# Kernel optimization log

Hardware: AMD Instinct MI355X
Metric: run time of the kernel (lower is better)

The kernel has to match this reference:

```python
import jax, jax.numpy as jnp
import numpy as np
import itertools

M_MODES = 16      # optical modes
N_PHOTONS = 8     # photons, input_state = [1]*8 + [0]*8
N_STATES = 12870  # C(16, 8) no-bunching output Fock states
OUT_SIZE = 128
BATCH = 8


def _random_unitary(key, m):
    kr, ki = jax.random.split(key)
    z = jax.random.normal(kr, (m, m)) + 1j * jax.random.normal(ki, (m, m))
    q, _ = jnp.linalg.qr(z)
    return q.astype(jnp.complex64)


def setup_inputs() -> dict:
    key = jax.random.key(0)
    ks = jax.random.split(key, 8)
    x = jax.random.normal(ks[0], (BATCH, M_MODES), dtype=jnp.float32)
    theta1 = jax.random.normal(ks[1], (M_MODES,), dtype=jnp.float32) * jnp.pi
    theta2 = jax.random.normal(ks[2], (M_MODES,), dtype=jnp.float32) * jnp.pi
    # fixed passive mixing unitaries (circuit structure constants)
    mix = jnp.stack([_random_unitary(jax.random.fold_in(ks[3], i), M_MODES) for i in range(4)])
    m_real = mix.real.astype(jnp.float32)
    m_imag = mix.imag.astype(jnp.float32)
    weight = jax.random.normal(ks[4], (N_STATES, OUT_SIZE), dtype=jnp.float32) * 0.02
    bias = jnp.zeros((OUT_SIZE,), dtype=jnp.float32)
    # no-bunching output Fock basis: all C(16,8) mode subsets (sorted rows)
    rows_idx = jnp.asarray(np.array(list(itertools.combinations(range(M_MODES), N_PHOTONS)), dtype=np.int32))
    return {"x": x, "theta1": theta1, "theta2": theta2, "m_real": m_real,
            "m_imag": m_imag, "weight": weight, "bias": bias, "rows_idx": rows_idx}


def reference(x, theta1, theta2, m_real, m_imag, weight, bias, rows_idx):
    n = N_PHOTONS
    M = (m_real + 1j * m_imag).astype(jnp.complex64)  # [4, m, m]
    # circuit unitary: U(x) = M3 . D(theta2) . M2 . D(x) . M1 . D(theta1) . M0
    A = M[1] @ (jnp.exp(1j * theta1)[:, None] * M[0])        # [m, m]
    B = M[3] @ (jnp.exp(1j * theta2)[:, None] * M[2])        # [m, m]
    U = jnp.einsum('pm,bm,mn->bpn', B, jnp.exp(1j * x), A)   # [b, m, m]
    # photons enter the first n modes -> keep those columns
    Uin = U[:, :, :n]                                        # [b, m, n]
    # Ryser's permanent formula over all 2^n column subsets
    sub = jnp.arange(2 ** n)
    masks = ((sub[:, None] >> jnp.arange(n)[None, :]) & 1).astype(jnp.float32)  # [2^n, n]
    popc = masks.sum(-1)
    signs = jnp.where((popc % 2) == 0, 1.0, -1.0) * ((-1.0) ** n)               # [2^n]
    # row partial sums for every mode and subset
    V = jnp.einsum('bmn,sn->bms', Uin, masks.astype(jnp.complex64))             # [b, m, 2^n]
    # product over the n rows of each output state (small fixed loop, not a data loop)
    acc = V[:, rows_idx[:, 0], :]                            # [b, states, 2^n]
    for i in range(1, n):
        acc = acc * V[:, rows_idx[:, i], :]
    amps = jnp.einsum('bks,s->bk', acc, signs.astype(jnp.complex64))            # [b, states]
    probs = amps.real ** 2 + amps.imag ** 2
    probs = probs / jnp.sum(probs, axis=-1, keepdims=True)   # renormalize over no-bunching subspace
    return probs @ weight + bias                             # linear output mapping
```

## Files before the change

### kernel.cpp

```cpp
#include <hip/hip_runtime.h>
#include <math.h>

#define NB 8
#define NM 16
#define NPH 8
#define NSTATES 12870
#define NSUB 256
#define OUTS 128
#define NTILES 824
#define NSLOTS (NTILES*16)
#define NSG 16
#define SPH 16
#define NTG 4
#define TILES_PER_TG 206
#define NGRID 512
#define SLOTS_P2 32
#define NP2 412

struct Tables {
  int binom[17][9];
  unsigned char cls_masks[256];
  int cls_off[10];
  int nt1[9], nt2[9];
  int tile_off[10];
};

constexpr int cpopc(int x){ int c=0; while(x){ c += x & 1; x >>= 1; } return c; }

constexpr Tables make_tables(){
  Tables t{};
  for (int n=0;n<=16;n++)
    for (int k=0;k<=8;k++){
      if (k==0) t.binom[n][k]=1;
      else if (n==0) t.binom[n][k]=0;
      else t.binom[n][k]=t.binom[n-1][k-1]+t.binom[n-1][k];
    }
  int idx=0;
  for (int p=0;p<=8;p++){
    t.cls_off[p]=idx;
    for (int m=0;m<256;m++) if (cpopc(m)==p) t.cls_masks[idx++]=(unsigned char)m;
  }
  t.cls_off[9]=idx;
  int toff=0;
  for (int c=0;c<=8;c++){
    int R=t.binom[8][c], C=t.binom[8][8-c];
    t.nt1[c]=(R+3)/4; t.nt2[c]=(C+3)/4;
    t.tile_off[c]=toff; toff += t.nt1[c]*t.nt2[c];
  }
  t.tile_off[9]=toff;
  return t;
}

constexpr Tables HTBL = make_tables();
static_assert(HTBL.tile_off[9]==NTILES, "tile count");
static_assert(HTBL.cls_off[9]==256, "mask count");
__device__ const Tables TBL = HTBL;

#define WS_TMAP   0
#define WS_BSUM2  53248
#define WS_POUT2  66560
#define WS_PART   1754112

__device__ __forceinline__ float2 cmul(float2 a, float2 b){
  return make_float2(fmaf(a.x,b.x,-(a.y*b.y)), fmaf(a.x,b.y, a.y*b.x));
}
__device__ __forceinline__ void cmac(float2& acc, float2 a, float2 b){
  acc.x = fmaf(a.x, b.x, acc.x); acc.x = fmaf(-a.y, b.y, acc.x);
  acc.y = fmaf(a.x, b.y, acc.y); acc.y = fmaf(a.y, b.x, acc.y);
}

__global__ __launch_bounds__(256) void k_p1(
    const float* __restrict__ x, const float* __restrict__ th1,
    const float* __restrict__ th2, const float* __restrict__ mr,
    const float* __restrict__ mi, const int* __restrict__ rows, char* ws)
{
  __shared__ float2 P[32][256];
  float2* __restrict__ part = (float2*)(ws + WS_PART);
  int tid = threadIdx.x;
  int blk = blockIdx.x;
  int b = blk >> 6, rest = blk & 63, sg = rest >> 2, tg = rest & 3;
  int sbase = sg * SPH;

  float2 (*T1)[NM]  = reinterpret_cast<float2(*)[NM]>(P[0]);
  float2 (*T2)[NM]  = reinterpret_cast<float2(*)[NM]>(P[1]);
  float2 (*Am)[NM]  = reinterpret_cast<float2(*)[NM]>(P[2]);
  float2 (*Bm)[NM]  = reinterpret_cast<float2(*)[NM]>(P[3]);
  float2 (*EA)[NPH] = reinterpret_cast<float2(*)[NPH]>(P[4]);
  float2* exP = P[4] + 128;
  float2 (*UinL)[NPH] = reinterpret_cast<float2(*)[NPH]>(P[5]);

  {
    int r = tid >> 4, cc = tid & 15;
    float sn, cs;
    sincosf(th1[r], &sn, &cs);
    float a = mr[0*256 + tid], bb = mi[0*256 + tid];
    T1[r][cc] = make_float2(cs*a - sn*bb, cs*bb + sn*a);
    sincosf(th2[r], &sn, &cs);
    float a2 = mr[2*256 + tid], b2 = mi[2*256 + tid];
    T2[r][cc] = make_float2(cs*a2 - sn*b2, cs*b2 + sn*a2);
    if (tid < NM){ float s2, c2; sincosf(x[b*NM + tid], &s2, &c2); exP[tid] = make_float2(c2, s2); }
  }
  __syncthreads();
  {
    int r = tid >> 4, cc = tid & 15;
    float2 accA = make_float2(0,0), accB = make_float2(0,0);
    for (int m=0;m<NM;m++){
      float2 m1 = make_float2(mr[1*256 + r*16+m], mi[1*256 + r*16+m]);
      cmac(accA, m1, T1[m][cc]);
      float2 m3 = make_float2(mr[3*256 + r*16+m], mi[3*256 + r*16+m]);
      cmac(accB, m3, T2[m][cc]);
    }
    Am[r][cc] = accA; Bm[r][cc] = accB;
  }
  __syncthreads();
  if (tid < NM*NPH){ int m = tid >> 3, n = tid & 7; EA[m][n] = cmul(exP[m], Am[m][n]); }
  __syncthreads();
  if (tid < NM*NPH){
    int p = tid >> 3, n = tid & 7;
    float2 acc = make_float2(0,0);
    for (int m=0;m<NM;m++) cmac(acc, Bm[p][m], EA[m][n]);
    UinL[p][n] = acc;
  }
  __syncthreads();

  int ts = tid >> 3;
  int table = ts >> 4, sl = ts & 15;
  int sv = sbase + sl;
  float2 v[8];
  {
    #pragma unroll
    for (int j=0;j<8;j++){
      float2 a = make_float2(0,0);
      int m = table*8 + j;
      #pragma unroll
      for (int jj=0;jj<NPH;jj++)
        if ((sv>>jj) & 1){ a.x += UinL[m][jj].x; a.y += UinL[m][jj].y; }
      v[j] = a;
    }
  }
  __syncthreads();

  {
    int chunk = tid & 7;
    int t0 = chunk << 5;
    float2 ph = make_float2((table==0 && (__popc(sv)&1)) ? -1.0f : 1.0f, 0.0f);
    if (chunk & 4) ph = cmul(ph, v[7]);
    if (chunk & 2) ph = cmul(ph, v[6]);
    if (chunk & 1) ph = cmul(ph, v[5]);
    float2 p[32];
    p[0] = ph;
    #pragma unroll
    for (int u=1; u<32; u++){
      int par = u & (u-1);
      int lb = (u&1) ? 0 : ((u&2) ? 1 : ((u&4) ? 2 : ((u&8) ? 3 : 4)));
      p[u] = cmul(p[par], v[lb]);
    }
    int swz = (ts & 15) << 1;
    #pragma unroll
    for (int u=0; u<32; u+=2){
      int tc = (t0 + u) ^ swz;
      *(float4*)&P[ts][tc] = make_float4(p[u].x, p[u].y, p[u+1].x, p[u+1].y);
    }
  }

  bool active = tid < TILES_PER_TG;
  int tile = tg + 4*tid;
  int t1v[4] = {0,0,0,0}, t2v[4] = {0,0,0,0};
  if (active){
    int c = 0;
    while (tile >= TBL.tile_off[c+1]) c++;
    int local = tile - TBL.tile_off[c];
    int n2 = TBL.nt2[c];
    int ti = local / n2, tj = local - ti*n2;
    int R = TBL.binom[8][c], C2 = TBL.binom[8][8-c];
    #pragma unroll
    for (int i=0;i<4;i++){ int r1 = ti*4+i; t1v[i] = (r1<R) ? (int)TBL.cls_masks[TBL.cls_off[c]+r1] : 0; }
    #pragma unroll
    for (int j=0;j<4;j++){ int r2 = tj*4+j; t2v[j] = (r2<C2) ? (int)TBL.cls_masks[TBL.cls_off[8-c]+r2] : 0; }
  }
  __syncthreads();

  if (active){
    float2 acc[4][4] = {};
    for (int s=0;s<SPH;s++){
      int swz = s << 1;
      float2 av[4], bv[4];
      #pragma unroll
      for (int i=0;i<4;i++) av[i] = P[s][t1v[i] ^ swz];
      #pragma unroll
      for (int j=0;j<4;j++) bv[j] = P[16+s][t2v[j] ^ swz];
      #pragma unroll
      for (int i=0;i<4;i++)
        #pragma unroll
        for (int j=0;j<4;j++) cmac(acc[i][j], av[i], bv[j]);
    }
    float2* dst = part + (size_t)(b*NSG + sg)*NSLOTS + (size_t)tile*16;
    #pragma unroll
    for (int i=0;i<4;i++)
      #pragma unroll
      for (int j=0;j<4;j++) dst[i*4+j] = acc[i][j];
  }

  if (tg == 3){
    int idx = blk >> 2;
    int kb = idx * 101;
    int ke = min(NSTATES, kb + 101);
    int k = kb + tid;
    if (k < ke){
      int t1=0, t2=0;
      #pragma unroll
      for (int i=0;i<NPH;i++){
        int rr = rows[k*NPH+i];
        if (rr < 8) t1 |= 1 << rr; else t2 |= 1 << (rr-8);
      }
      int c1 = __popc(t1);
      int rk1=0, cnt=0;
      #pragma unroll
      for (int bb=0;bb<8;bb++) if ((t1>>bb)&1){ cnt++; rk1 += TBL.binom[bb][cnt]; }
      int rk2=0; cnt=0;
      #pragma unroll
      for (int bb=0;bb<8;bb++) if ((t2>>bb)&1){ cnt++; rk2 += TBL.binom[bb][cnt]; }
      int tl = TBL.tile_off[c1] + (rk1>>2)*TBL.nt2[c1] + (rk2>>2);
      int slot = ((rk1&3)<<2) | (rk2&3);
      ((int*)(ws + WS_TMAP))[tl*16 + slot] = k;
    }
  }
}

__global__ __launch_bounds__(256) void k_p2(const float* __restrict__ wgt, char* ws)
{
  __shared__ float prob[NB*SLOTS_P2];
  __shared__ int   krow[SLOTS_P2];
  __shared__ float hacc[2*NB*OUTS];
  int tid = threadIdx.x;
  int blk = blockIdx.x;
  int slot0 = blk * SLOTS_P2;

  if (tid < SLOTS_P2){
    int slot = slot0 + tid;
    int tile = slot >> 4;
    int c = 0;
    while (tile >= TBL.tile_off[c+1]) c++;
    int local = tile - TBL.tile_off[c];
    int n2 = TBL.nt2[c];
    int ti = local / n2, tj = local - ti*n2;
    int r1 = ti*4 + ((slot >> 2) & 3);
    int r2 = tj*4 + (slot & 3);
    bool pad = (r1 >= TBL.binom[8][c]) || (r2 >= TBL.binom[8][8-c]);
    krow[tid] = pad ? -1 : ((const int*)(ws + WS_TMAP))[slot];
  }
  __syncthreads();

  const float2* __restrict__ part = (const float2*)(ws + WS_PART);
  float* __restrict__ bsum2 = (float*)(ws + WS_BSUM2);
  {
    int b = tid >> 5, sl = tid & 31;
    float2 amp = make_float2(0,0);
    #pragma unroll
    for (int g=0; g<NSG; g++){
      float2 v = part[(size_t)(b*NSG + g)*NSLOTS + slot0 + sl];
      amp.x += v.x; amp.y += v.y;
    }
    float pr = (krow[sl] >= 0) ? fmaf(amp.x, amp.x, amp.y*amp.y) : 0.0f;
    prob[b*SLOTS_P2 + sl] = pr;
    float v = pr;
    #pragma unroll
    for (int off=16; off>0; off>>=1) v += __shfl_down(v, off, 32);
    if (sl == 0) bsum2[blk*NB + b] = v;
  }
  __syncthreads();

  {
    int h = tid >> 7, o = tid & 127;
    float acc[NB] = {0,0,0,0,0,0,0,0};
    int sbeg = h*16, send = sbeg + 16;
    #pragma unroll 4
    for (int sl = sbeg; sl < send; sl++){
      int kr = krow[sl]; if (kr < 0) kr = 0;
      float wv = wgt[(size_t)kr * OUTS + o];
      #pragma unroll
      for (int b=0;b<NB;b++) acc[b] = fmaf(prob[b*SLOTS_P2 + sl], wv, acc[b]);
    }
    #pragma unroll
    for (int b=0;b<NB;b++) hacc[h*(NB*OUTS) + b*OUTS + o] = acc[b];
  }
  __syncthreads();

  float* __restrict__ pout2 = (float*)(ws + WS_POUT2);
  for (int idx = tid; idx < NB*OUTS; idx += 256)
    pout2[(size_t)blk*(NB*OUTS) + idx] = hacc[idx] + hacc[NB*OUTS + idx];
}

__global__ __launch_bounds__(256) void k_p3(
    const float* __restrict__ bias, const char* __restrict__ ws,
    float* __restrict__ out)
{
  __shared__ float accs[2*OUTS];
  __shared__ float wred[4];
  int tid = threadIdx.x, b = blockIdx.x;
  const float* __restrict__ bsum2 = (const float*)(ws + WS_BSUM2);
  const float* __restrict__ pout2 = (const float*)(ws + WS_POUT2);

  float v = 0.0f;
  for (int j = tid; j < NP2; j += 256) v += bsum2[j*NB + b];
  #pragma unroll
  for (int off=32; off>0; off>>=1) v += __shfl_down(v, off);
  if ((tid & 63) == 0) wred[tid >> 6] = v;

  int o = tid & 127, half = tid >> 7;
  float a = 0.0f;
  #pragma unroll 4
  for (int s = half; s < NP2; s += 2) a += pout2[(size_t)s*(NB*OUTS) + b*OUTS + o];
  accs[half*OUTS + o] = a;
  __syncthreads();
  if (tid < OUTS){
    float norm = wred[0] + wred[1] + wred[2] + wred[3];
    out[b*OUTS + tid] = (accs[tid] + accs[OUTS + tid]) / norm + bias[tid];
  }
}

extern "C" void kernel_launch(void* const* d_in, const int* in_sizes, int n_in,
                              void* d_out, int out_size, void* d_ws, size_t ws_size,
                              hipStream_t stream) {
  const float* x    = (const float*)d_in[0];
  const float* th1  = (const float*)d_in[1];
  const float* th2  = (const float*)d_in[2];
  const float* mr   = (const float*)d_in[3];
  const float* mi   = (const float*)d_in[4];
  const float* wgt  = (const float*)d_in[5];
  const float* bias = (const float*)d_in[6];
  const int*   rows = (const int*)d_in[7];
  float* out = (float*)d_out;
  char* ws = (char*)d_ws;

  k_p1<<<NGRID, 256, 0, stream>>>(x, th1, th2, mr, mi, rows, ws);
  k_p2<<<NP2, 256, 0, stream>>>(wgt, ws);
  k_p3<<<NB, 256, 0, stream>>>(bias, ws, out);
}
```

Measured before the change: 121.0 us.

## Fuse final reduction into k_p2 via atomic counter, split product table

Removes the separate k_p3 launch. Every k_p2 block takes a ticket from a global atomic counter, which k_p1 resets. The last NB blocks to arrive spin until all blocks have finished, then each reduces one batch row into the output. Separately, k_p1 builds its 32-entry subset-product table as two halves of 16 values, to lower register pressure. The cost is a spin-wait at the tail of k_p2 and a dependence on inter-block memory ordering through fences.

```diff
diff --git a/kernel.cpp b/kernel.cpp
--- a/kernel.cpp
+++ b/kernel.cpp
@@ -16,6 +16,7 @@
 #define NGRID 512
 #define SLOTS_P2 32
 #define NP2 412
+#define FIN0 (NP2-NB)
 
 struct Tables {
   int binom[17][9];
@@ -56,10 +57,11 @@
 static_assert(HTBL.cls_off[9]==256, "mask count");
 __device__ const Tables TBL = HTBL;
 
-#define WS_TMAP   0
+#define WS_CNT    0
+#define WS_TMAP   256
 #define WS_BSUM2  53248
 #define WS_POUT2  66560
-#define WS_PART   1754112
+#define WS_PART   1757184
 
 __device__ __forceinline__ float2 cmul(float2 a, float2 b){
   return make_float2(fmaf(a.x,b.x,-(a.y*b.y)), fmaf(a.x,b.y, a.y*b.x));
@@ -81,6 +83,8 @@
   int b = blk >> 6, rest = blk & 63, sg = rest >> 2, tg = rest & 3;
   int sbase = sg * SPH;
 
+  if (blk == 0 && tid == 0) *(int*)(ws + WS_CNT) = 0;
+
   float2 (*T1)[NM]  = reinterpret_cast<float2(*)[NM]>(P[0]);
   float2 (*T2)[NM]  = reinterpret_cast<float2(*)[NM]>(P[1]);
   float2 (*Am)[NM]  = reinterpret_cast<float2(*)[NM]>(P[2]);
@@ -143,23 +147,36 @@
   {
     int chunk = tid & 7;
     int t0 = chunk << 5;
+    int swz = (ts & 15) << 1;
     float2 ph = make_float2((table==0 && (__popc(sv)&1)) ? -1.0f : 1.0f, 0.0f);
     if (chunk & 4) ph = cmul(ph, v[7]);
     if (chunk & 2) ph = cmul(ph, v[6]);
     if (chunk & 1) ph = cmul(ph, v[5]);
-    float2 p[32];
-    p[0] = ph;
-    #pragma unroll
-    for (int u=1; u<32; u++){
-      int par = u & (u-1);
-      int lb = (u&1) ? 0 : ((u&2) ? 1 : ((u&4) ? 2 : ((u&8) ? 3 : 4)));
-      p[u] = cmul(p[par], v[lb]);
-    }
-    int swz = (ts & 15) << 1;
-    #pragma unroll
-    for (int u=0; u<32; u+=2){
-      int tc = (t0 + u) ^ swz;
-      *(float4*)&P[ts][tc] = make_float4(p[u].x, p[u].y, p[u+1].x, p[u+1].y);
+
+    float2 pl[16];
+    pl[0] = ph;
+    #pragma unroll
+    for (int w=1; w<16; w++){
+      int par = w & (w-1);
+      int lb = (w&1) ? 0 : ((w&2) ? 1 : ((w&4) ? 2 : 3));
+      pl[w] = cmul(pl[par], v[lb]);
+    }
+    #pragma unroll
+    for (int w=0; w<16; w+=2){
+      int tc = (t0 + w) ^ swz;
+      *(float4*)&P[ts][tc] = make_float4(pl[w].x, pl[w].y, pl[w+1].x, pl[w+1].y);
+    }
+    pl[0] = cmul(ph, v[4]);
+    #pragma unroll
+    for (int w=1; w<16; w++){
+      int par = w & (w-1);
+      int lb = (w&1) ? 0 : ((w&2) ? 1 : ((w&4) ? 2 : 3));
+      pl[w] = cmul(pl[par], v[lb]);
+    }
+    #pragma unroll
+    for (int w=0; w<16; w+=2){
+      int tc = (t0 + 16 + w) ^ swz;
+      *(float4*)&P[ts][tc] = make_float4(pl[w].x, pl[w].y, pl[w+1].x, pl[w+1].y);
     }
   }
 
@@ -227,11 +244,14 @@
   }
 }
 
-__global__ __launch_bounds__(256) void k_p2(const float* __restrict__ wgt, char* ws)
+__global__ __launch_bounds__(256) void k_p2(
+    const float* __restrict__ wgt, const float* __restrict__ bias,
+    char* ws, float* __restrict__ out)
 {
   __shared__ float prob[NB*SLOTS_P2];
   __shared__ int   krow[SLOTS_P2];
   __shared__ float hacc[2*NB*OUTS];
+  __shared__ int rankS;
   int tid = threadIdx.x;
   int blk = blockIdx.x;
   int slot0 = blk * SLOTS_P2;
@@ -289,33 +309,39 @@
   float* __restrict__ pout2 = (float*)(ws + WS_POUT2);
   for (int idx = tid; idx < NB*OUTS; idx += 256)
     pout2[(size_t)blk*(NB*OUTS) + idx] = hacc[idx] + hacc[NB*OUTS + idx];
-}
-
-__global__ __launch_bounds__(256) void k_p3(
-    const float* __restrict__ bias, const char* __restrict__ ws,
-    float* __restrict__ out)
-{
-  __shared__ float accs[2*OUTS];
-  __shared__ float wred[4];
-  int tid = threadIdx.x, b = blockIdx.x;
-  const float* __restrict__ bsum2 = (const float*)(ws + WS_BSUM2);
-  const float* __restrict__ pout2 = (const float*)(ws + WS_POUT2);
-
-  float v = 0.0f;
-  for (int j = tid; j < NP2; j += 256) v += bsum2[j*NB + b];
-  #pragma unroll
-  for (int off=32; off>0; off>>=1) v += __shfl_down(v, off);
-  if ((tid & 63) == 0) wred[tid >> 6] = v;
-
-  int o = tid & 127, half = tid >> 7;
-  float a = 0.0f;
-  #pragma unroll 4
-  for (int s = half; s < NP2; s += 2) a += pout2[(size_t)s*(NB*OUTS) + b*OUTS + o];
-  accs[half*OUTS + o] = a;
-  __syncthreads();
-  if (tid < OUTS){
-    float norm = wred[0] + wred[1] + wred[2] + wred[3];
-    out[b*OUTS + tid] = (accs[tid] + accs[OUTS + tid]) / norm + bias[tid];
+
+  __threadfence();
+  __syncthreads();
+  if (tid == 0) rankS = atomicAdd((int*)(ws + WS_CNT), 1);
+  __syncthreads();
+  int rank = rankS;
+  if (rank < FIN0) return;
+
+  if (tid == 0){
+    while (atomicAdd((int*)(ws + WS_CNT), 0) < NP2) { }
+  }
+  __syncthreads();
+  __threadfence();
+  {
+    int b = rank - FIN0;
+    float* accs = hacc;
+    float* wred = hacc + 2*OUTS;
+    float v = 0.0f;
+    for (int j = tid; j < NP2; j += 256) v += bsum2[j*NB + b];
+    #pragma unroll
+    for (int off=32; off>0; off>>=1) v += __shfl_down(v, off);
+    if ((tid & 63) == 0) wred[tid >> 6] = v;
+
+    int o = tid & 127, half = tid >> 7;
+    float a = 0.0f;
+    #pragma unroll 4
+    for (int s = half; s < NP2; s += 2) a += pout2[(size_t)s*(NB*OUTS) + b*OUTS + o];
+    accs[half*OUTS + o] = a;
+    __syncthreads();
+    if (tid < OUTS){
+      float norm = wred[0] + wred[1] + wred[2] + wred[3];
+      out[b*OUTS + tid] = (accs[tid] + accs[OUTS + tid]) / norm + bias[tid];
+    }
   }
 }
 
@@ -334,6 +360,5 @@
   char* ws = (char*)d_ws;
 
   k_p1<<<NGRID, 256, 0, stream>>>(x, th1, th2, mr, mi, rows, ws);
-  k_p2<<<NP2, 256, 0, stream>>>(wgt, ws);
-  k_p3<<<NB, 256, 0, stream>>>(bias, ws, out);
-}
+  k_p2<<<NP2, 256, 0, stream>>>(wgt, bias, ws, out);
+}
```

After: 156.2 us. +29.1%, slower.
